# Kernel optimization log

Measured on AMD Instinct MI355X. Metric: run time of the kernel, lower is better.

The kernel has to match this reference:

```python
import jax, jax.numpy as jnp
import numpy as np

NUM_KERNELS = 8
KERNEL_SIZES = [2 ** i for i in range(1, NUM_KERNELS + 1)]


def setup_inputs() -> dict:
    key = jax.random.key(0)
    x = jax.random.uniform(key, (32, 1, 1024, 1024), dtype=jnp.float32)
    return {"x": x}


def _plogp(p):
    # p * log2(p), safely 0 at p == 0 (log2(1) == 0)
    ps = jnp.where(p > 0, p, 1.0)
    return ps * jnp.log2(ps)


def reference(x):
    # Slice_windows(num_kernels=8, mode='entropy', to_binary=False)
    B, C, H, W = x.shape
    cols = []
    for k in KERNEL_SIZES:
        if k > H or k > W:
            cols.append(jnp.zeros((B,), dtype=x.dtype))
            continue
        Hk, Wk = H // k, W // k
        n = k * k * C
        # non-overlapping window sums == sum-pooling with stride k
        xs = x[:, :, : Hk * k, : Wk * k].reshape(B, C, Hk, k, Wk, k)
        s = xs.sum(axis=(1, 3, 5))            # (B, Hk, Wk)
        p1 = s / n
        p0 = 1.0 - p1
        entropy = -_plogp(p0) - _plogp(p1)    # Shannon entropy per window
        cols.append(entropy.mean(axis=(1, 2)))  # average over all windows
    return jnp.stack(cols, axis=1)  # (B, num_kernels)
```

## Files before the change

### kernel.cpp

```cpp
#include <hip/hip_runtime.h>

#define IMG 1024

__device__ __forceinline__ float ent(float s, float inv_n) {
    float p1 = s * inv_n;
    float p0 = 1.0f - p1;
    float l1 = (p1 > 0.0f) ? __log2f(p1) : 0.0f;
    float l0 = (p0 > 0.0f) ? __log2f(p0) : 0.0f;
    return -(p0 * l0 + p1 * l1);
}

__device__ __forceinline__ float bfly_sum(float v) {
#pragma unroll
    for (int m = 32; m >= 1; m >>= 1) v += __shfl_xor(v, m);
    return v;
}

__global__ __launch_bounds__(256, 4) void slice_k1(const float* __restrict__ x,
                                                   float* __restrict__ ws) {
    const int b    = blockIdx.x >> 6;
    const int tile = blockIdx.x & 63;
    const int tr = tile >> 3, tc = tile & 7;
    const int t = threadIdx.x;
    const int w = t >> 6, lane = t & 63;
    const int wr = w >> 1, wc = w & 1;
    const int cy = lane >> 3, cx = lane & 7;

    const int row0 = tr * 128 + wr * 64 + cy * 8;
    const int col0 = tc * 128 + wc * 64 + cx * 8;
    const float* p = x + (size_t)b * (IMG * IMG) + (size_t)row0 * IMG + col0;

    float4 va[8], vb[8];
#pragma unroll
    for (int i = 0; i < 8; ++i) {
        va[i] = *(const float4*)(p + (size_t)i * IMG);
        vb[i] = *(const float4*)(p + (size_t)i * IMG + 4);
    }

    float e2sum = 0.f, e4sum = 0.f;
    float s4[2][2] = {{0.f, 0.f}, {0.f, 0.f}};
#pragma unroll
    for (int ry = 0; ry < 4; ++ry) {
        float4 a0 = va[2 * ry], a1 = va[2 * ry + 1];
        float4 b0 = vb[2 * ry], b1 = vb[2 * ry + 1];
        float sA = a0.x + a0.y + a1.x + a1.y;
        float sB = a0.z + a0.w + a1.z + a1.w;
        float sC = b0.x + b0.y + b1.x + b1.y;
        float sD = b0.z + b0.w + b1.z + b1.w;
        e2sum += ent(sA, 0.25f) + ent(sB, 0.25f) + ent(sC, 0.25f) + ent(sD, 0.25f);
        s4[ry >> 1][0] += sA + sB;
        s4[ry >> 1][1] += sC + sD;
    }
    float s8 = 0.f;
#pragma unroll
    for (int i = 0; i < 2; ++i)
#pragma unroll
        for (int j = 0; j < 2; ++j) { e4sum += ent(s4[i][j], 1.f / 16.f); s8 += s4[i][j]; }
    float e8 = ent(s8, 1.f / 64.f);

    float s16 = s8 + __shfl_xor(s8, 1);  s16 += __shfl_xor(s16, 8);
    float e16 = ent(s16, 1.f / 256.f);
    float s32 = s16 + __shfl_xor(s16, 2); s32 += __shfl_xor(s32, 16);
    float e32 = ent(s32, 1.f / 1024.f);
    float s64 = s32 + __shfl_xor(s32, 4); s64 += __shfl_xor(s64, 32);
    float e64 = ent(s64, 1.f / 4096.f);

    float E2 = bfly_sum(e2sum);
    float E4 = bfly_sum(e4sum);
    float E8 = bfly_sum(e8);
    float E16 = e16 + __shfl_xor(e16, 2); E16 += __shfl_xor(E16, 4);
    E16 += __shfl_xor(E16, 16);   E16 += __shfl_xor(E16, 32);
    float E32 = e32 + __shfl_xor(e32, 4); E32 += __shfl_xor(E32, 32);

    __shared__ float wl[4][8];
    if (lane == 0) {
        wl[w][0] = E2;  wl[w][1] = E4;  wl[w][2] = E8;
        wl[w][3] = E16; wl[w][4] = E32; wl[w][5] = e64; wl[w][6] = s64;
    }
    __syncthreads();
    if (t < 8) {
        float r;
        if (t < 6) {
            r = wl[0][t] + wl[1][t] + wl[2][t] + wl[3][t];
        } else {
            float s128 = wl[0][6] + wl[1][6] + wl[2][6] + wl[3][6];
            r = (t == 6) ? ent(s128, 1.f / 16384.f) : s128;
        }
        ws[(size_t)blockIdx.x * 8 + t] = r;
    }
}

__global__ __launch_bounds__(64) void slice_k2(const float* __restrict__ ws,
                                               float* __restrict__ out) {
    const int b = blockIdx.x, l = threadIdx.x;
    const float4* g = (const float4*)(ws + ((size_t)b * 64 + l) * 8);
    float4 u0 = g[0], u1 = g[1];
    float v[8] = {u0.x, u0.y, u0.z, u0.w, u1.x, u1.y, u1.z, u1.w};

    float s256 = v[7] + __shfl_xor(v[7], 1); s256 += __shfl_xor(s256, 8);
    float e256 = ent(s256, 1.f / 65536.f);
    float E256 = e256 + __shfl_xor(e256, 2); E256 += __shfl_xor(E256, 4);
    E256 += __shfl_xor(E256, 16);  E256 += __shfl_xor(E256, 32);

    float sums[7];
#pragma unroll
    for (int j = 0; j < 7; ++j) sums[j] = bfly_sum(v[j]);

    if (l == 0) {
        const float invw[7] = {1.f / 262144.f, 1.f / 65536.f, 1.f / 16384.f,
                               1.f / 4096.f,   1.f / 1024.f,  1.f / 256.f, 1.f / 64.f};
        float* o = out + b * 8;
#pragma unroll
        for (int j = 0; j < 7; ++j) o[j] = sums[j] * invw[j];
        o[7] = E256 * (1.f / 16.f);
    }
}

extern "C" void kernel_launch(void* const* d_in, const int* in_sizes, int n_in,
                              void* d_out, int out_size, void* d_ws, size_t ws_size,
                              hipStream_t stream) {
    const float* x = (const float*)d_in[0];
    float* out = (float*)d_out;
    float* ws  = (float*)d_ws;

    slice_k1<<<32 * 64, 256, 0, stream>>>(x, ws);
    slice_k2<<<32, 64, 0, stream>>>(ws, out);
}
```

Baseline: 184.6 us.

## Remap thread tiles to row-contiguous float4 strips with shuffle-based window sums

Each wavefront now covers 32 rows of the 128x128 tile. Every lane reads one float4 per row, so 32 lanes span a full 512-byte row segment, replacing the earlier 8x8 per-lane patches. Row pairs are combined through a cross-half shuffle, and larger windows are built by combining register sums and shuffles, with 64-window sums gathered in shared memory. The aim is fully coalesced loads. The cost is more shuffles per element and duplicated entropy work in both half-waves, with the double counting undone by scale factors.

Result: slower. 190.3 us (+3.1%).

```diff
diff --git a/kernel.cpp b/kernel.cpp
--- a/kernel.cpp
+++ b/kernel.cpp
@@ -23,68 +23,80 @@
     const int tr = tile >> 3, tc = tile & 7;
     const int t = threadIdx.x;
     const int w = t >> 6, lane = t & 63;
-    const int wr = w >> 1, wc = w & 1;
-    const int cy = lane >> 3, cx = lane & 7;
+    const int hi = lane >> 5, lo = lane & 31;
 
-    const int row0 = tr * 128 + wr * 64 + cy * 8;
-    const int col0 = tc * 128 + wc * 64 + cx * 8;
-    const float* p = x + (size_t)b * (IMG * IMG) + (size_t)row0 * IMG + col0;
+    const float* p = x + (size_t)b * (IMG * IMG)
+                       + (size_t)(tr * 128 + w * 32 + hi) * IMG + (tc * 128 + lo * 4);
 
-    float4 va[8], vb[8];
+    float4 v[16];
 #pragma unroll
-    for (int i = 0; i < 8; ++i) {
-        va[i] = *(const float4*)(p + (size_t)i * IMG);
-        vb[i] = *(const float4*)(p + (size_t)i * IMG + 4);
+    for (int i = 0; i < 16; ++i)
+        v[i] = *(const float4*)(p + (size_t)(2 * i) * IMG);
+
+    float e2 = 0.f, e4 = 0.f, e8 = 0.f, e16 = 0.f;
+    float s4p[16];
+#pragma unroll
+    for (int i = 0; i < 16; ++i) {
+        float h0 = v[i].x + v[i].y;
+        float h1 = v[i].z + v[i].w;
+        float s2a = h0 + __shfl_xor(h0, 32);
+        float s2b = h1 + __shfl_xor(h1, 32);
+        e2 += ent(s2a, 0.25f) + ent(s2b, 0.25f);
+        s4p[i] = s2a + s2b;
     }
+    float s4[8], s8[4], s16[2];
+#pragma unroll
+    for (int j = 0; j < 8; ++j) {
+        s4[j] = s4p[2 * j] + s4p[2 * j + 1];
+        e4 += ent(s4[j], 1.f / 16.f);
+    }
+#pragma unroll
+    for (int m = 0; m < 4; ++m) {
+        float t8 = s4[2 * m] + s4[2 * m + 1];
+        s8[m] = t8 + __shfl_xor(t8, 1);
+        e8 += ent(s8[m], 1.f / 64.f);
+    }
+#pragma unroll
+    for (int q = 0; q < 2; ++q) {
+        float t16 = s8[2 * q] + s8[2 * q + 1];
+        s16[q] = t16 + __shfl_xor(t16, 2);
+        e16 += ent(s16[q], 1.f / 256.f);
+    }
+    float t32 = s16[0] + s16[1];
+    float s32 = t32 + __shfl_xor(t32, 4);
+    float e32 = ent(s32, 1.f / 1024.f);
 
-    float e2sum = 0.f, e4sum = 0.f;
-    float s4[2][2] = {{0.f, 0.f}, {0.f, 0.f}};
-#pragma unroll
-    for (int ry = 0; ry < 4; ++ry) {
-        float4 a0 = va[2 * ry], a1 = va[2 * ry + 1];
-        float4 b0 = vb[2 * ry], b1 = vb[2 * ry + 1];
-        float sA = a0.x + a0.y + a1.x + a1.y;
-        float sB = a0.z + a0.w + a1.z + a1.w;
-        float sC = b0.x + b0.y + b1.x + b1.y;
-        float sD = b0.z + b0.w + b1.z + b1.w;
-        e2sum += ent(sA, 0.25f) + ent(sB, 0.25f) + ent(sC, 0.25f) + ent(sD, 0.25f);
-        s4[ry >> 1][0] += sA + sB;
-        s4[ry >> 1][1] += sC + sD;
+    float E2  = bfly_sum(e2);
+    float E4  = bfly_sum(e4);
+    float E8  = bfly_sum(e8);
+    float E16 = bfly_sum(e16);
+    float E32 = bfly_sum(e32);
+
+    __shared__ float wl[4][5];
+    __shared__ float wl32[4][4];
+    if (lane == 0) {
+        wl[w][0] = E2 * 0.5f;   wl[w][1] = E4 * 0.5f;  wl[w][2] = E8 * 0.25f;
+        wl[w][3] = E16 * 0.125f; wl[w][4] = E32 * 0.0625f;
     }
-    float s8 = 0.f;
-#pragma unroll
-    for (int i = 0; i < 2; ++i)
-#pragma unroll
-        for (int j = 0; j < 2; ++j) { e4sum += ent(s4[i][j], 1.f / 16.f); s8 += s4[i][j]; }
-    float e8 = ent(s8, 1.f / 64.f);
+    if (hi == 0 && (lo & 7) == 0) wl32[w][lo >> 3] = s32;
+    __syncthreads();
 
-    float s16 = s8 + __shfl_xor(s8, 1);  s16 += __shfl_xor(s16, 8);
-    float e16 = ent(s16, 1.f / 256.f);
-    float s32 = s16 + __shfl_xor(s16, 2); s32 += __shfl_xor(s32, 16);
-    float e32 = ent(s32, 1.f / 1024.f);
-    float s64 = s32 + __shfl_xor(s32, 4); s64 += __shfl_xor(s64, 32);
-    float e64 = ent(s64, 1.f / 4096.f);
-
-    float E2 = bfly_sum(e2sum);
-    float E4 = bfly_sum(e4sum);
-    float E8 = bfly_sum(e8);
-    float E16 = e16 + __shfl_xor(e16, 2); E16 += __shfl_xor(E16, 4);
-    E16 += __shfl_xor(E16, 16);   E16 += __shfl_xor(E16, 32);
-    float E32 = e32 + __shfl_xor(e32, 4); E32 += __shfl_xor(E32, 32);
-
-    __shared__ float wl[4][8];
-    if (lane == 0) {
-        wl[w][0] = E2;  wl[w][1] = E4;  wl[w][2] = E8;
-        wl[w][3] = E16; wl[w][4] = E32; wl[w][5] = e64; wl[w][6] = s64;
-    }
-    __syncthreads();
     if (t < 8) {
         float r;
-        if (t < 6) {
+        if (t < 5) {
             r = wl[0][t] + wl[1][t] + wl[2][t] + wl[3][t];
         } else {
-            float s128 = wl[0][6] + wl[1][6] + wl[2][6] + wl[3][6];
-            r = (t == 6) ? ent(s128, 1.f / 16384.f) : s128;
+            float s64a = wl32[0][0] + wl32[0][1] + wl32[1][0] + wl32[1][1];
+            float s64b = wl32[0][2] + wl32[0][3] + wl32[1][2] + wl32[1][3];
+            float s64c = wl32[2][0] + wl32[2][1] + wl32[3][0] + wl32[3][1];
+            float s64d = wl32[2][2] + wl32[2][3] + wl32[3][2] + wl32[3][3];
+            if (t == 5) {
+                r = ent(s64a, 1.f / 4096.f) + ent(s64b, 1.f / 4096.f)
+                  + ent(s64c, 1.f / 4096.f) + ent(s64d, 1.f / 4096.f);
+            } else {
+                float s128 = s64a + s64b + s64c + s64d;
+                r = (t == 6) ? ent(s128, 1.f / 16384.f) : s128;
+            }
         }
         ws[(size_t)blockIdx.x * 8 + t] = r;
     }
```

## Retile pyramid reduction into 32x256 strips with LDS combine and finer blocks

Applied to the files above, without the earlier changes.

Each block now covers a 32x256 strip with 4 waves, and each thread loads one float4 per row across 8 rows (8 loads instead of 16). This gives fully coalesced 1 KB row segments per wave. Mid-level window sums (16, 32) are combined through shared memory, and the 64/128/256 levels move to a larger second kernel that holds the per-image 32x32 grid of s32 sums in LDS. The intent is better coalescing, lower register pressure (launch bounds 8), and twice as many blocks, at the cost of more LDS traffic and a heavier finalisation kernel.

Measured after the change: 185.6 us. No clear change (+0.6%).

```diff
diff --git a/kernel.cpp b/kernel.cpp
--- a/kernel.cpp
+++ b/kernel.cpp
@@ -16,103 +16,126 @@
     return v;
 }
 
-__global__ __launch_bounds__(256, 4) void slice_k1(const float* __restrict__ x,
+__global__ __launch_bounds__(256, 8) void slice_k1(const float* __restrict__ x,
                                                    float* __restrict__ ws) {
-    const int b    = blockIdx.x >> 6;
-    const int tile = blockIdx.x & 63;
-    const int tr = tile >> 3, tc = tile & 7;
+    const int b    = blockIdx.x >> 7;
+    const int tile = blockIdx.x & 127;
+    const int R = tile >> 2, C = tile & 3;
     const int t = threadIdx.x;
-    const int w = t >> 6, lane = t & 63;
-    const int wr = w >> 1, wc = w & 1;
-    const int cy = lane >> 3, cx = lane & 7;
+    const int w = t >> 6, l = t & 63;
 
-    const int row0 = tr * 128 + wr * 64 + cy * 8;
-    const int col0 = tc * 128 + wc * 64 + cx * 8;
-    const float* p = x + (size_t)b * (IMG * IMG) + (size_t)row0 * IMG + col0;
+    const float* p = x + (size_t)b * (IMG * IMG)
+                       + (size_t)(R * 32 + w * 8) * IMG + (C * 256 + l * 4);
+    float4 v[8];
+#pragma unroll
+    for (int i = 0; i < 8; ++i)
+        v[i] = *(const float4*)(p + (size_t)i * IMG);
 
-    float4 va[8], vb[8];
+    float e2 = 0.f, e4 = 0.f;
+    float s4h[4];
 #pragma unroll
-    for (int i = 0; i < 8; ++i) {
-        va[i] = *(const float4*)(p + (size_t)i * IMG);
-        vb[i] = *(const float4*)(p + (size_t)i * IMG + 4);
+    for (int i = 0; i < 4; ++i) {
+        float4 a = v[2 * i], c = v[2 * i + 1];
+        float s2a = a.x + a.y + c.x + c.y;
+        float s2b = a.z + a.w + c.z + c.w;
+        e2 += ent(s2a, 0.25f) + ent(s2b, 0.25f);
+        s4h[i] = s2a + s2b;
     }
-
-    float e2sum = 0.f, e4sum = 0.f;
-    float s4[2][2] = {{0.f, 0.f}, {0.f, 0.f}};
-#pragma unroll
-    for (int ry = 0; ry < 4; ++ry) {
-        float4 a0 = va[2 * ry], a1 = va[2 * ry + 1];
-        float4 b0 = vb[2 * ry], b1 = vb[2 * ry + 1];
-        float sA = a0.x + a0.y + a1.x + a1.y;
-        float sB = a0.z + a0.w + a1.z + a1.w;
-        float sC = b0.x + b0.y + b1.x + b1.y;
-        float sD = b0.z + b0.w + b1.z + b1.w;
-        e2sum += ent(sA, 0.25f) + ent(sB, 0.25f) + ent(sC, 0.25f) + ent(sD, 0.25f);
-        s4[ry >> 1][0] += sA + sB;
-        s4[ry >> 1][1] += sC + sD;
-    }
-    float s8 = 0.f;
-#pragma unroll
-    for (int i = 0; i < 2; ++i)
-#pragma unroll
-        for (int j = 0; j < 2; ++j) { e4sum += ent(s4[i][j], 1.f / 16.f); s8 += s4[i][j]; }
+    float s4a = s4h[0] + s4h[1], s4b = s4h[2] + s4h[3];
+    e4 = ent(s4a, 1.f / 16.f) + ent(s4b, 1.f / 16.f);
+    float t8 = s4a + s4b;
+    float s8 = t8 + __shfl_xor(t8, 1);
     float e8 = ent(s8, 1.f / 64.f);
 
-    float s16 = s8 + __shfl_xor(s8, 1);  s16 += __shfl_xor(s16, 8);
-    float e16 = ent(s16, 1.f / 256.f);
-    float s32 = s16 + __shfl_xor(s16, 2); s32 += __shfl_xor(s32, 16);
-    float e32 = ent(s32, 1.f / 1024.f);
-    float s64 = s32 + __shfl_xor(s32, 4); s64 += __shfl_xor(s64, 32);
-    float e64 = ent(s64, 1.f / 4096.f);
+    float E2 = bfly_sum(e2), E4 = bfly_sum(e4), E8 = bfly_sum(e8);
 
-    float E2 = bfly_sum(e2sum);
-    float E4 = bfly_sum(e4sum);
-    float E8 = bfly_sum(e8);
-    float E16 = e16 + __shfl_xor(e16, 2); E16 += __shfl_xor(E16, 4);
-    E16 += __shfl_xor(E16, 16);   E16 += __shfl_xor(E16, 32);
-    float E32 = e32 + __shfl_xor(e32, 4); E32 += __shfl_xor(E32, 32);
+    __shared__ float s8l[4][32];
+    __shared__ float wle[4][3];
+    if ((l & 1) == 0) s8l[w][l >> 1] = s8;
+    if (l == 0) { wle[w][0] = E2; wle[w][1] = E4; wle[w][2] = E8 * 0.5f; }
+    __syncthreads();
 
-    __shared__ float wl[4][8];
-    if (lane == 0) {
-        wl[w][0] = E2;  wl[w][1] = E4;  wl[w][2] = E8;
-        wl[w][3] = E16; wl[w][4] = E32; wl[w][5] = e64; wl[w][6] = s64;
-    }
-    __syncthreads();
-    if (t < 8) {
-        float r;
-        if (t < 6) {
-            r = wl[0][t] + wl[1][t] + wl[2][t] + wl[3][t];
-        } else {
-            float s128 = wl[0][6] + wl[1][6] + wl[2][6] + wl[3][6];
-            r = (t == 6) ? ent(s128, 1.f / 16384.f) : s128;
+    if (w == 0) {
+        int r = (l >> 4) & 1, c = l & 15;
+        float s16 = s8l[2 * r][2 * c]     + s8l[2 * r][2 * c + 1]
+                  + s8l[2 * r + 1][2 * c] + s8l[2 * r + 1][2 * c + 1];
+        float e16 = ent(s16, 1.f / 256.f);
+        float u = s16 + __shfl_xor(s16, 1);
+        float s32 = u + __shfl_xor(u, 16);
+        float e32 = ent(s32, 1.f / 1024.f);
+        float E16 = bfly_sum(e16) * 0.5f;
+        float E32 = bfly_sum(e32) * 0.125f;
+        if (l < 16 && (l & 1) == 0)
+            ws[(size_t)b * 1024 + R * 32 + C * 8 + (l >> 1)] = s32;
+        if (l == 0) {
+            float* rec = ws + 32768 + (size_t)blockIdx.x * 8;
+            rec[0] = wle[0][0] + wle[1][0] + wle[2][0] + wle[3][0];
+            rec[1] = wle[0][1] + wle[1][1] + wle[2][1] + wle[3][1];
+            rec[2] = wle[0][2] + wle[1][2] + wle[2][2] + wle[3][2];
+            rec[3] = E16;
+            rec[4] = E32;
         }
-        ws[(size_t)blockIdx.x * 8 + t] = r;
     }
 }
 
-__global__ __launch_bounds__(64) void slice_k2(const float* __restrict__ ws,
-                                               float* __restrict__ out) {
-    const int b = blockIdx.x, l = threadIdx.x;
-    const float4* g = (const float4*)(ws + ((size_t)b * 64 + l) * 8);
-    float4 u0 = g[0], u1 = g[1];
-    float v[8] = {u0.x, u0.y, u0.z, u0.w, u1.x, u1.y, u1.z, u1.w};
+__global__ __launch_bounds__(256) void slice_k2(const float* __restrict__ ws,
+                                                float* __restrict__ out) {
+    const int b = blockIdx.x, t = threadIdx.x;
+    const int w = t >> 6, l = t & 63;
 
-    float s256 = v[7] + __shfl_xor(v[7], 1); s256 += __shfl_xor(s256, 8);
-    float e256 = ent(s256, 1.f / 65536.f);
-    float E256 = e256 + __shfl_xor(e256, 2); E256 += __shfl_xor(E256, 4);
-    E256 += __shfl_xor(E256, 16);  E256 += __shfl_xor(E256, 32);
+    __shared__ float g[1024];
+    ((float4*)g)[t] = ((const float4*)(ws + (size_t)b * 1024))[t];
 
-    float sums[7];
-#pragma unroll
-    for (int j = 0; j < 7; ++j) sums[j] = bfly_sum(v[j]);
+    float r0 = 0.f, r1 = 0.f, r2 = 0.f, r3 = 0.f, r4 = 0.f;
+    if (t < 128) {
+        const float* rec = ws + 32768 + ((size_t)(b * 128 + t)) * 8;
+        float4 a = *(const float4*)rec;
+        r0 = a.x; r1 = a.y; r2 = a.z; r3 = a.w; r4 = rec[4];
+    }
+    r0 = bfly_sum(r0); r1 = bfly_sum(r1); r2 = bfly_sum(r2);
+    r3 = bfly_sum(r3); r4 = bfly_sum(r4);
+    __shared__ float wr[4][5];
+    __shared__ float w64s[4];
+    __shared__ float l64[256];
+    if (l == 0) { wr[w][0] = r0; wr[w][1] = r1; wr[w][2] = r2; wr[w][3] = r3; wr[w][4] = r4; }
+    __syncthreads();
 
-    if (l == 0) {
-        const float invw[7] = {1.f / 262144.f, 1.f / 65536.f, 1.f / 16384.f,
-                               1.f / 4096.f,   1.f / 1024.f,  1.f / 256.f, 1.f / 64.f};
-        float* o = out + b * 8;
-#pragma unroll
-        for (int j = 0; j < 7; ++j) o[j] = sums[j] * invw[j];
-        o[7] = E256 * (1.f / 16.f);
+    int i = t >> 4, j = t & 15;
+    float s64 = g[(2 * i) * 32 + 2 * j]     + g[(2 * i) * 32 + 2 * j + 1]
+              + g[(2 * i + 1) * 32 + 2 * j] + g[(2 * i + 1) * 32 + 2 * j + 1];
+    float e64 = ent(s64, 1.f / 4096.f);
+    l64[t] = s64;
+    float E64w = bfly_sum(e64);
+    if (l == 0) w64s[w] = E64w;
+    __syncthreads();
+
+    if (w == 0) {
+        int i2 = l >> 3, j2 = l & 7;
+        float s128 = l64[(2 * i2) * 16 + 2 * j2]     + l64[(2 * i2) * 16 + 2 * j2 + 1]
+                   + l64[(2 * i2 + 1) * 16 + 2 * j2] + l64[(2 * i2 + 1) * 16 + 2 * j2 + 1];
+        float e128 = ent(s128, 1.f / 16384.f);
+        float E128 = bfly_sum(e128);
+        float u = s128 + __shfl_xor(s128, 1);
+        float s256 = u + __shfl_xor(u, 8);
+        float e256 = ent(s256, 1.f / 65536.f);
+        float E256 = bfly_sum(e256) * 0.25f;
+        if (l == 0) {
+            float E2 = wr[0][0] + wr[1][0] + wr[2][0] + wr[3][0];
+            float E4 = wr[0][1] + wr[1][1] + wr[2][1] + wr[3][1];
+            float E8 = wr[0][2] + wr[1][2] + wr[2][2] + wr[3][2];
+            float E16 = wr[0][3] + wr[1][3] + wr[2][3] + wr[3][3];
+            float E32 = wr[0][4] + wr[1][4] + wr[2][4] + wr[3][4];
+            float E64 = w64s[0] + w64s[1] + w64s[2] + w64s[3];
+            float* o = out + b * 8;
+            o[0] = E2  * (1.f / 262144.f);
+            o[1] = E4  * (1.f / 65536.f);
+            o[2] = E8  * (1.f / 16384.f);
+            o[3] = E16 * (1.f / 4096.f);
+            o[4] = E32 * (1.f / 1024.f);
+            o[5] = E64 * (1.f / 256.f);
+            o[6] = E128 * (1.f / 64.f);
+            o[7] = E256 * (1.f / 16.f);
+        }
     }
 }
 
@@ -123,6 +146,6 @@
     float* out = (float*)d_out;
     float* ws  = (float*)d_ws;
 
-    slice_k1<<<32 * 64, 256, 0, stream>>>(x, ws);
-    slice_k2<<<32, 64, 0, stream>>>(ws, out);
+    slice_k1<<<32 * 128, 256, 0, stream>>>(x, ws);
+    slice_k2<<<32, 256, 0, stream>>>(ws, out);
 }
```
